# Kernel tuning notes

Hardware: AMD Instinct MI355X
Metric: run time of the kernel (lower is better)

## Reference

```python
import jax, jax.numpy as jnp
import numpy as np

D_IN = 1024
D_OUT = 1024
NUM_HEADS = 16
HEAD_DIM = D_OUT // NUM_HEADS


def setup_inputs() -> dict:
    key = jax.random.key(0)
    ks = jax.random.split(key, 6)
    s = 0.02
    return {
        "x": jax.random.normal(ks[0], (4, 2048, D_IN), dtype=jnp.float32),
        "Wq": jax.random.normal(ks[1], (D_IN, D_OUT), dtype=jnp.float32) * s,
        "Wk": jax.random.normal(ks[2], (D_IN, D_OUT), dtype=jnp.float32) * s,
        "Wv": jax.random.normal(ks[3], (D_IN, D_OUT), dtype=jnp.float32) * s,
        "Wo": jax.random.normal(ks[4], (D_OUT, D_OUT), dtype=jnp.float32) * s,
        "bo": jax.random.normal(ks[5], (D_OUT,), dtype=jnp.float32) * s,
    }


def reference(x, Wq, Wk, Wv, Wo, bo):
    b, n, _ = x.shape
    h, hd = NUM_HEADS, HEAD_DIM
    # project and split heads: (b, h, n, hd)
    q = (x @ Wq).reshape(b, n, h, hd).transpose(0, 2, 1, 3)
    k = (x @ Wk).reshape(b, n, h, hd).transpose(0, 2, 1, 3)
    v = (x @ Wv).reshape(b, n, h, hd).transpose(0, 2, 1, 3)
    scores = jnp.einsum("bhqd,bhkd->bhqk", q, k)
    causal = jnp.triu(jnp.ones((n, n), dtype=bool), k=1)  # True above diagonal
    scores = jnp.where(causal, -jnp.inf, scores)
    attn = jax.nn.softmax(scores / jnp.sqrt(jnp.float32(hd)), axis=-1)
    ctx = jnp.einsum("bhqk,bhkd->bhqd", attn, v)
    ctx = ctx.transpose(0, 2, 1, 3).reshape(b, n, h * hd)
    return ctx @ Wo + bo
```

## Files before the change

### kernel.cpp

```cpp
#include <hip/hip_runtime.h>

#define DEV __device__ __forceinline__

typedef unsigned short u16;
typedef unsigned int u32;
typedef __attribute__((ext_vector_type(8))) short short8;
typedef __attribute__((ext_vector_type(4))) float floatx4;

DEV u16 f2bf(float f) {
  union { float f; unsigned u; } v; v.f = f;
  return (u16)((v.u + 0x7FFFu + ((v.u >> 16) & 1u)) >> 16);
}
DEV u32 fbits(float f) { union { float f; u32 u; } v; v.f = f; return v.u; }

DEV void gl2lds16(const void* g, void* l) {
  __builtin_amdgcn_global_load_lds((const __attribute__((address_space(1))) void*)g,
                                   (__attribute__((address_space(3))) void*)l, 16, 0, 0);
}

__global__ void cvt_f32_bf16_x4(const float* __restrict__ in, u16* __restrict__ out, int n4) {
  int i = blockIdx.x * blockDim.x + threadIdx.x;
  if (i >= n4) return;
  float4 f = ((const float4*)in)[i];
  ushort4 o;
  o.x = f2bf(f.x); o.y = f2bf(f.y); o.z = f2bf(f.z); o.w = f2bf(f.w);
  ((ushort4*)out)[i] = o;
}

__global__ void transpose_f32_bf16(const float* __restrict__ W, u16* __restrict__ Wt) {
  __shared__ float t[32][33];
  int tx = threadIdx.x & 31, ty = threadIdx.x >> 5;
  int x0 = blockIdx.x * 32, y0 = blockIdx.y * 32;
#pragma unroll
  for (int i = 0; i < 32; i += 8)
    t[ty + i][tx] = W[(size_t)(y0 + ty + i) * 1024 + x0 + tx];
  __syncthreads();
#pragma unroll
  for (int i = 0; i < 32; i += 8)
    Wt[(size_t)(x0 + ty + i) * 1024 + y0 + tx] = f2bf(t[tx][ty + i]);
}

__global__ __launch_bounds__(256, 4)
void gemm_qkv(const u16* __restrict__ A, const u16* __restrict__ Bt,
              u16* __restrict__ Qo, u16* __restrict__ Ko, u16* __restrict__ Vto,
              float alpha) {
  __shared__ u16 smem[16384];
  u16* As = smem;
  u16* Bs = smem + 8192;
  const int tid = threadIdx.x;
  const int wave = tid >> 6, lane = tid & 63;
  const int quad = lane >> 4, l16 = lane & 15, l7 = l16 & 7;
  const int n0 = blockIdx.x * 128, m0 = blockIdx.y * 128;
  const int wm = (wave >> 1) * 64, wn = (wave & 1) * 64;

  floatx4 acc[4][4] = {};
  const int sl = lane >> 3;
  const int sp = lane & 7;
  for (int kt = 0; kt < 1024; kt += 64) {
    __syncthreads();
#pragma unroll
    for (int it = 0; it < 4; ++it) {
      int g = it * 4 + wave;
      int row = g * 8 + sl;
      int lc = (sp ^ (row & 7)) * 8;
      gl2lds16(&A[(size_t)(m0 + row) * 1024 + kt + lc], &As[g * 512]);
      gl2lds16(&Bt[(size_t)(n0 + row) * 1024 + kt + lc], &Bs[g * 512]);
    }
    __syncthreads();
#pragma unroll
    for (int ks = 0; ks < 2; ++ks) {
      const int rc = ((ks * 4 + quad) ^ l7) * 8;
      short8 ar[4], br[4];
#pragma unroll
      for (int i = 0; i < 4; ++i)
        ar[i] = *(const short8*)&As[(wm + i * 16 + l16) * 64 + rc];
#pragma unroll
      for (int j = 0; j < 4; ++j)
        br[j] = *(const short8*)&Bs[(wn + j * 16 + l16) * 64 + rc];
#pragma unroll
      for (int i = 0; i < 4; ++i)
#pragma unroll
        for (int j = 0; j < 4; ++j)
          acc[i][j] = __builtin_amdgcn_mfma_f32_16x16x32_bf16(ar[i], br[j], acc[i][j], 0, 0, 0);
    }
  }

  if (n0 < 1024) {
#pragma unroll
    for (int i = 0; i < 4; ++i) {
      int row = m0 + wm + i * 16 + quad * 4;
#pragma unroll
      for (int j = 0; j < 4; ++j) {
        int col = n0 + wn + j * 16 + l16;
#pragma unroll
        for (int r = 0; r < 4; ++r)
          Qo[(size_t)(row + r) * 1024 + col] = f2bf(acc[i][j][r] * alpha);
      }
    }
  } else if (n0 < 2048) {
#pragma unroll
    for (int i = 0; i < 4; ++i) {
      int row = m0 + wm + i * 16 + quad * 4;
#pragma unroll
      for (int j = 0; j < 4; ++j) {
        int col = n0 - 1024 + wn + j * 16 + l16;
#pragma unroll
        for (int r = 0; r < 4; ++r)
          Ko[(size_t)(row + r) * 1024 + col] = f2bf(acc[i][j][r]);
      }
    }
  } else {
    __syncthreads();
#pragma unroll
    for (int i = 0; i < 4; ++i) {
      int rowrel0 = wm + i * 16 + quad * 4;
#pragma unroll
      for (int j = 0; j < 4; ++j) {
        int colrel = wn + j * 16 + l16;
        ushort4 pk;
        pk.x = f2bf(acc[i][j][0]); pk.y = f2bf(acc[i][j][1]);
        pk.z = f2bf(acc[i][j][2]); pk.w = f2bf(acc[i][j][3]);
        *(ushort4*)&smem[colrel * 128 + (rowrel0 ^ ((colrel & 15) * 8))] = pk;
      }
    }
    __syncthreads();
    const int bb = m0 >> 11, q0r = m0 & 2047;
    const int fl = tid >> 4, qp = (tid & 15) * 8;
#pragma unroll
    for (int p = 0; p < 8; ++p) {
      int f = p * 16 + fl;
      int col = n0 - 2048 + f;
      int h = col >> 6, d = col & 63;
      int sw = (f & 15) * 8;
      uint2 lo = *(const uint2*)&smem[f * 128 + (qp ^ sw)];
      uint2 hi = *(const uint2*)&smem[f * 128 + ((qp + 4) ^ sw)];
      uint4 val = make_uint4(lo.x, lo.y, hi.x, hi.y);
      *(uint4*)&Vto[(size_t)(((bb * 16 + h) * 64 + d)) * 2048 + q0r + qp] = val;
    }
  }
}

__global__ __launch_bounds__(256, 4)
void gemm_out(const u16* __restrict__ A, const u16* __restrict__ Bt,
              float* __restrict__ C, const float* __restrict__ bias) {
  __shared__ u16 smem[16384];
  u16* As = smem;
  u16* Bs = smem + 8192;
  const int tid = threadIdx.x;
  const int wave = tid >> 6, lane = tid & 63;
  const int quad = lane >> 4, l16 = lane & 15, l7 = l16 & 7;
  const int n0 = blockIdx.x * 128, m0 = blockIdx.y * 128;
  const int wm = (wave >> 1) * 64, wn = (wave & 1) * 64;

  floatx4 acc[4][4] = {};
  const int sl = lane >> 3;
  const int sp = lane & 7;

  for (int kt = 0; kt < 1024; kt += 64) {
    __syncthreads();
#pragma unroll
    for (int it = 0; it < 4; ++it) {
      int g = it * 4 + wave;
      int row = g * 8 + sl;
      int lc = (sp ^ (row & 7)) * 8;
      gl2lds16(&A[(size_t)(m0 + row) * 1024 + kt + lc], &As[g * 512]);
      gl2lds16(&Bt[(size_t)(n0 + row) * 1024 + kt + lc], &Bs[g * 512]);
    }
    __syncthreads();
#pragma unroll
    for (int ks = 0; ks < 2; ++ks) {
      const int rc = ((ks * 4 + quad) ^ l7) * 8;
      short8 ar[4], br[4];
#pragma unroll
      for (int i = 0; i < 4; ++i)
        ar[i] = *(const short8*)&As[(wm + i * 16 + l16) * 64 + rc];
#pragma unroll
      for (int j = 0; j < 4; ++j)
        br[j] = *(const short8*)&Bs[(wn + j * 16 + l16) * 64 + rc];
#pragma unroll
      for (int i = 0; i < 4; ++i)
#pragma unroll
        for (int j = 0; j < 4; ++j)
          acc[i][j] = __builtin_amdgcn_mfma_f32_16x16x32_bf16(ar[i], br[j], acc[i][j], 0, 0, 0);
    }
  }
#pragma unroll
  for (int j = 0; j < 4; ++j) {
    int col = n0 + wn + j * 16 + l16;
    float bj = bias[col];
#pragma unroll
    for (int i = 0; i < 4; ++i) {
      int row = m0 + wm + i * 16 + quad * 4;
#pragma unroll
      for (int r = 0; r < 4; ++r)
        C[(size_t)(row + r) * 1024 + col] = acc[i][j][r] + bj;
    }
  }
}

__global__ __launch_bounds__(256)
void flash_attn(const u16* __restrict__ Qg, const u16* __restrict__ Kg,
                const u16* __restrict__ Vtg, u16* __restrict__ ctx) {
  __shared__ u16 Qs[128 * 64];
  __shared__ u16 Ks[64 * 64];
  __shared__ u16 Vs[64 * 64];
  __shared__ u16 Ps[4][32 * 64];
  const int tid = threadIdx.x;
  const int wave = tid >> 6, lane = tid & 63;
  const int quad = lane >> 4, l16 = lane & 15, l7 = l16 & 7;
  const int bh = blockIdx.y, b = bh >> 4, h = bh & 15;
  const size_t qkbase = (size_t)b * 2048 * 1024 + (size_t)h * 64;
  const size_t vbase = (size_t)bh * 64 * 2048;
  const int sl = lane >> 3, sp = lane & 7;
  u16* Pw = &Ps[wave][0];

  for (int phase = 0; phase < 2; ++phase) {
    const int qt = phase == 0 ? (15 - (int)blockIdx.x) : (int)blockIdx.x;
    const int q0 = qt * 128;
    __syncthreads();
    {
#pragma unroll
      for (int it = 0; it < 4; ++it) {
        int g = it * 4 + wave;
        int r = g * 8 + sl;
        int lc = (sp ^ (r & 7)) * 8;
        gl2lds16(&Qg[qkbase + (size_t)(q0 + r) * 1024 + lc], &Qs[g * 512]);
      }
    }
    float lsum[2] = {0.f, 0.f};
    floatx4 o[4][2] = {};

    const int qbase = q0 + wave * 32;
    const int nt = 2 * qt + 2;

    for (int t = 0; t < nt; ++t) {
      const int kv0 = t * 64;
      __syncthreads();
      {
#pragma unroll
        for (int it = 0; it < 2; ++it) {
          int g = it * 4 + wave;
          int r = g * 8 + sl;
          int lc = (sp ^ (r & 7)) * 8;
          gl2lds16(&Kg[qkbase + (size_t)(kv0 + r) * 1024 + lc], &Ks[g * 512]);
          gl2lds16(&Vtg[vbase + (size_t)r * 2048 + kv0 + lc], &Vs[g * 512]);
        }
      }
      __syncthreads();

      if (kv0 > qbase + 31) continue;

      floatx4 st[4][2] = {};
#pragma unroll
      for (int ks = 0; ks < 2; ++ks) {
        const int rc = ((ks * 4 + quad) ^ l7) * 8;
        short8 ak[4], bq[2];
#pragma unroll
        for (int mj = 0; mj < 4; ++mj)
          ak[mj] = *(const short8*)&Ks[(mj * 16 + l16) * 64 + rc];
#pragma unroll
        for (int qi = 0; qi < 2; ++qi)
          bq[qi] = *(const short8*)&Qs[(wave * 32 + qi * 16 + l16) * 64 + rc];
#pragma unroll
        for (int mj = 0; mj < 4; ++mj)
#pragma unroll
          for (int qi = 0; qi < 2; ++qi)
            st[mj][qi] = __builtin_amdgcn_mfma_f32_16x16x32_bf16(ak[mj], bq[qi], st[mj][qi], 0, 0, 0);
      }
#pragma unroll
      for (int mj = 0; mj < 4; ++mj)
#pragma unroll
        for (int qi = 0; qi < 2; ++qi)
#pragma unroll
          for (int r = 0; r < 4; ++r)
            st[mj][qi][r] = __builtin_amdgcn_exp2f(st[mj][qi][r]);
      if (kv0 + 63 > qbase) {
#pragma unroll
        for (int mj = 0; mj < 4; ++mj)
#pragma unroll
          for (int r = 0; r < 4; ++r) {
            int gk = kv0 + mj * 16 + quad * 4 + r;
#pragma unroll
            for (int qi = 0; qi < 2; ++qi) {
              int gq = qbase + qi * 16 + l16;
              if (gk > gq) st[mj][qi][r] = 0.f;
            }
          }
      }
#pragma unroll
      for (int mj = 0; mj < 4; ++mj)
#pragma unroll
        for (int qi = 0; qi < 2; ++qi)
          lsum[qi] += (st[mj][qi][0] + st[mj][qi][1]) + (st[mj][qi][2] + st[mj][qi][3]);
#pragma unroll
      for (int qi = 0; qi < 2; ++qi) {
        int rowoff = (qi * 16 + l16) * 64;
#pragma unroll
        for (int mj = 0; mj < 4; ++mj) {
          u32 lo = __builtin_amdgcn_perm(fbits(st[mj][qi][1]), fbits(st[mj][qi][0]), 0x07060302u);
          u32 hi = __builtin_amdgcn_perm(fbits(st[mj][qi][3]), fbits(st[mj][qi][2]), 0x07060302u);
          int off = rowoff + (((mj * 2 + (quad >> 1)) ^ l7) << 3) + (quad & 1) * 4;
          *(uint2*)&Pw[off] = make_uint2(lo, hi);
        }
      }
#pragma unroll
      for (int ks = 0; ks < 2; ++ks) {
        const int rc = ((ks * 4 + quad) ^ l7) * 8;
        short8 av[4], bp[2];
#pragma unroll
        for (int dj = 0; dj < 4; ++dj)
          av[dj] = *(const short8*)&Vs[(dj * 16 + l16) * 64 + rc];
#pragma unroll
        for (int qi = 0; qi < 2; ++qi)
          bp[qi] = *(const short8*)&Pw[(qi * 16 + l16) * 64 + rc];
#pragma unroll
        for (int dj = 0; dj < 4; ++dj)
#pragma unroll
          for (int qi = 0; qi < 2; ++qi)
            o[dj][qi] = __builtin_amdgcn_mfma_f32_16x16x32_bf16(av[dj], bp[qi], o[dj][qi], 0, 0, 0);
      }
    }
#pragma unroll
    for (int qi = 0; qi < 2; ++qi) {
      float tsum = lsum[qi];
      tsum += __shfl_xor(tsum, 16);
      tsum += __shfl_xor(tsum, 32);
      float inv = 1.f / tsum;
      int gq = qbase + qi * 16 + l16;
      size_t rowoff = ((size_t)b * 2048 + gq) * 1024 + (size_t)h * 64 + quad * 4;
#pragma unroll
      for (int dj = 0; dj < 4; ++dj) {
        ushort4 pk;
        pk.x = f2bf(o[dj][qi][0] * inv); pk.y = f2bf(o[dj][qi][1] * inv);
        pk.z = f2bf(o[dj][qi][2] * inv); pk.w = f2bf(o[dj][qi][3] * inv);
        *(ushort4*)&ctx[rowoff + dj * 16] = pk;
      }
    }
  }
}

extern "C" void kernel_launch(void* const* d_in, const int* in_sizes, int n_in,
                              void* d_out, int out_size, void* d_ws, size_t ws_size,
                              hipStream_t stream) {
  const float* x  = (const float*)d_in[0];
  const float* Wq = (const float*)d_in[1];
  const float* Wk = (const float*)d_in[2];
  const float* Wv = (const float*)d_in[3];
  const float* Wo = (const float*)d_in[4];
  const float* bo = (const float*)d_in[5];
  float* out = (float*)d_out;

  char* ws = (char*)d_ws;
  const size_t MB = (size_t)1 << 20;
  u16* x16    = (u16*)(ws + 0 * MB);
  u16* q16    = (u16*)(ws + 16 * MB);
  u16* k16    = (u16*)(ws + 32 * MB);
  u16* vt16   = (u16*)(ws + 48 * MB);
  u16* c16    = (u16*)(ws + 64 * MB);
  u16* wqkvt  = (u16*)(ws + 80 * MB);
  u16* wot    = (u16*)(ws + 86 * MB);

  const float sc2 = 0.125f * 1.44269504089f;

  cvt_f32_bf16_x4<<<8192, 256, 0, stream>>>(x, x16, 8192 * 1024 / 4);
  dim3 tg(32, 32);
  transpose_f32_bf16<<<tg, 256, 0, stream>>>(Wq, wqkvt);
  transpose_f32_bf16<<<tg, 256, 0, stream>>>(Wk, wqkvt + (size_t)1024 * 1024);
  transpose_f32_bf16<<<tg, 256, 0, stream>>>(Wv, wqkvt + (size_t)2048 * 1024);
  transpose_f32_bf16<<<tg, 256, 0, stream>>>(Wo, wot);

  dim3 g3(3072 / 128, 8192 / 128);
  gemm_qkv<<<g3, 256, 0, stream>>>(x16, wqkvt, q16, k16, vt16, sc2);

  dim3 ag(8, 64);
  flash_attn<<<ag, 256, 0, stream>>>(q16, k16, vt16, c16);

  dim3 gO(1024 / 128, 8192 / 128);
  gemm_out<<<gO, 256, 0, stream>>>(c16, wot, out, bo);
}
```

Baseline: 259.3 us.

## Use 128-wide KV tiles in flash attention and remap block indices for locality

Doubles the K/V tile from 64 to 128 keys per iteration, halving the number of load/sync rounds per query tile and computing 8 score subtiles per step. The V tile gets a wider 16-way XOR swizzle, and P is written and consumed in two 64-key halves through the existing per-wave LDS buffer. The 1D grid is remapped so neighbouring blocks share batch-heads, launch bounds request 2 blocks per CU, and the per-wave skip of fully masked tiles is dropped. In exchange, each wave now does some fully masked work on the diagonal tile, and LDS and register use rise.

```diff
diff --git a/kernel.cpp b/kernel.cpp
--- a/kernel.cpp
+++ b/kernel.cpp
@@ -198,24 +198,28 @@
   }
 }
 
-__global__ __launch_bounds__(256)
+__global__ __launch_bounds__(256, 2)
 void flash_attn(const u16* __restrict__ Qg, const u16* __restrict__ Kg,
                 const u16* __restrict__ Vtg, u16* __restrict__ ctx) {
   __shared__ u16 Qs[128 * 64];
-  __shared__ u16 Ks[64 * 64];
-  __shared__ u16 Vs[64 * 64];
+  __shared__ u16 Ks[128 * 64];
+  __shared__ u16 Vs[64 * 128];
   __shared__ u16 Ps[4][32 * 64];
   const int tid = threadIdx.x;
   const int wave = tid >> 6, lane = tid & 63;
   const int quad = lane >> 4, l16 = lane & 15, l7 = l16 & 7;
-  const int bh = blockIdx.y, b = bh >> 4, h = bh & 15;
+  const int bx = blockIdx.x;
+  const int p = (bx >> 3) & 7;
+  const int bh = (bx >> 6) * 8 + (bx & 7);
+  const int b = bh >> 4, h = bh & 15;
   const size_t qkbase = (size_t)b * 2048 * 1024 + (size_t)h * 64;
   const size_t vbase = (size_t)bh * 64 * 2048;
   const int sl = lane >> 3, sp = lane & 7;
+  const int sv = lane >> 4, sq = lane & 15;
   u16* Pw = &Ps[wave][0];
 
   for (int phase = 0; phase < 2; ++phase) {
-    const int qt = phase == 0 ? (15 - (int)blockIdx.x) : (int)blockIdx.x;
+    const int qt = phase == 0 ? (15 - p) : p;
     const int q0 = qt * 128;
     __syncthreads();
     {
@@ -231,52 +235,49 @@
     floatx4 o[4][2] = {};
 
     const int qbase = q0 + wave * 32;
-    const int nt = 2 * qt + 2;
+    const int nt = qt + 1;
 
     for (int t = 0; t < nt; ++t) {
-      const int kv0 = t * 64;
+      const int kv0 = t * 128;
       __syncthreads();
       {
 #pragma unroll
-        for (int it = 0; it < 2; ++it) {
+        for (int it = 0; it < 4; ++it) {
           int g = it * 4 + wave;
-          int r = g * 8 + sl;
-          int lc = (sp ^ (r & 7)) * 8;
-          gl2lds16(&Kg[qkbase + (size_t)(kv0 + r) * 1024 + lc], &Ks[g * 512]);
-          gl2lds16(&Vtg[vbase + (size_t)r * 2048 + kv0 + lc], &Vs[g * 512]);
+          int rk = g * 8 + sl;
+          int lck = (sp ^ (rk & 7)) * 8;
+          gl2lds16(&Kg[qkbase + (size_t)(kv0 + rk) * 1024 + lck], &Ks[g * 512]);
+          int rv = g * 4 + sv;
+          int lcv = (sq ^ (rv & 15)) * 8;
+          gl2lds16(&Vtg[vbase + (size_t)rv * 2048 + kv0 + lcv], &Vs[g * 512]);
         }
       }
       __syncthreads();
 
-      if (kv0 > qbase + 31) continue;
-
-      floatx4 st[4][2] = {};
+      floatx4 st[8][2] = {};
 #pragma unroll
       for (int ks = 0; ks < 2; ++ks) {
         const int rc = ((ks * 4 + quad) ^ l7) * 8;
-        short8 ak[4], bq[2];
-#pragma unroll
-        for (int mj = 0; mj < 4; ++mj)
-          ak[mj] = *(const short8*)&Ks[(mj * 16 + l16) * 64 + rc];
-#pragma unroll
-        for (int qi = 0; qi < 2; ++qi)
-          bq[qi] = *(const short8*)&Qs[(wave * 32 + qi * 16 + l16) * 64 + rc];
-#pragma unroll
-        for (int mj = 0; mj < 4; ++mj)
-#pragma unroll
-          for (int qi = 0; qi < 2; ++qi)
-            st[mj][qi] = __builtin_amdgcn_mfma_f32_16x16x32_bf16(ak[mj], bq[qi], st[mj][qi], 0, 0, 0);
-      }
-#pragma unroll
-      for (int mj = 0; mj < 4; ++mj)
+        short8 bq[2];
+        bq[0] = *(const short8*)&Qs[(wave * 32 + l16) * 64 + rc];
+        bq[1] = *(const short8*)&Qs[(wave * 32 + 16 + l16) * 64 + rc];
+#pragma unroll
+        for (int mj = 0; mj < 8; ++mj) {
+          short8 ak = *(const short8*)&Ks[(mj * 16 + l16) * 64 + rc];
+          st[mj][0] = __builtin_amdgcn_mfma_f32_16x16x32_bf16(ak, bq[0], st[mj][0], 0, 0, 0);
+          st[mj][1] = __builtin_amdgcn_mfma_f32_16x16x32_bf16(ak, bq[1], st[mj][1], 0, 0, 0);
+        }
+      }
+#pragma unroll
+      for (int mj = 0; mj < 8; ++mj)
 #pragma unroll
         for (int qi = 0; qi < 2; ++qi)
 #pragma unroll
           for (int r = 0; r < 4; ++r)
             st[mj][qi][r] = __builtin_amdgcn_exp2f(st[mj][qi][r]);
-      if (kv0 + 63 > qbase) {
-#pragma unroll
-        for (int mj = 0; mj < 4; ++mj)
+      if (t == nt - 1) {
+#pragma unroll
+        for (int mj = 0; mj < 8; ++mj)
 #pragma unroll
           for (int r = 0; r < 4; ++r) {
             int gk = kv0 + mj * 16 + quad * 4 + r;
@@ -288,36 +289,42 @@
           }
       }
 #pragma unroll
-      for (int mj = 0; mj < 4; ++mj)
+      for (int mj = 0; mj < 8; ++mj)
 #pragma unroll
         for (int qi = 0; qi < 2; ++qi)
           lsum[qi] += (st[mj][qi][0] + st[mj][qi][1]) + (st[mj][qi][2] + st[mj][qi][3]);
 #pragma unroll
-      for (int qi = 0; qi < 2; ++qi) {
-        int rowoff = (qi * 16 + l16) * 64;
-#pragma unroll
-        for (int mj = 0; mj < 4; ++mj) {
-          u32 lo = __builtin_amdgcn_perm(fbits(st[mj][qi][1]), fbits(st[mj][qi][0]), 0x07060302u);
-          u32 hi = __builtin_amdgcn_perm(fbits(st[mj][qi][3]), fbits(st[mj][qi][2]), 0x07060302u);
-          int off = rowoff + (((mj * 2 + (quad >> 1)) ^ l7) << 3) + (quad & 1) * 4;
-          *(uint2*)&Pw[off] = make_uint2(lo, hi);
+      for (int half = 0; half < 2; ++half) {
+#pragma unroll
+        for (int qi = 0; qi < 2; ++qi) {
+          int rowoff = (qi * 16 + l16) * 64;
+#pragma unroll
+          for (int mj2 = 0; mj2 < 4; ++mj2) {
+            int mj = half * 4 + mj2;
+            u32 lo = __builtin_amdgcn_perm(fbits(st[mj][qi][1]), fbits(st[mj][qi][0]), 0x07060302u);
+            u32 hi = __builtin_amdgcn_perm(fbits(st[mj][qi][3]), fbits(st[mj][qi][2]), 0x07060302u);
+            int off = rowoff + (((mj2 * 2 + (quad >> 1)) ^ l7) << 3) + (quad & 1) * 4;
+            *(uint2*)&Pw[off] = make_uint2(lo, hi);
+          }
         }
-      }
-#pragma unroll
-      for (int ks = 0; ks < 2; ++ks) {
-        const int rc = ((ks * 4 + quad) ^ l7) * 8;
-        short8 av[4], bp[2];
-#pragma unroll
-        for (int dj = 0; dj < 4; ++dj)
-          av[dj] = *(const short8*)&Vs[(dj * 16 + l16) * 64 + rc];
-#pragma unroll
-        for (int qi = 0; qi < 2; ++qi)
-          bp[qi] = *(const short8*)&Pw[(qi * 16 + l16) * 64 + rc];
-#pragma unroll
-        for (int dj = 0; dj < 4; ++dj)
+#pragma unroll
+        for (int ks2 = 0; ks2 < 2; ++ks2) {
+          const int ks = half * 2 + ks2;
+          const int rcv = ((ks * 4 + quad) ^ l16) * 8;
+          const int rcp = ((ks2 * 4 + quad) ^ l7) * 8;
+          short8 av[4], bp[2];
+#pragma unroll
+          for (int dj = 0; dj < 4; ++dj)
+            av[dj] = *(const short8*)&Vs[(dj * 16 + l16) * 128 + rcv];
 #pragma unroll
           for (int qi = 0; qi < 2; ++qi)
-            o[dj][qi] = __builtin_amdgcn_mfma_f32_16x16x32_bf16(av[dj], bp[qi], o[dj][qi], 0, 0, 0);
+            bp[qi] = *(const short8*)&Pw[(qi * 16 + l16) * 64 + rcp];
+#pragma unroll
+          for (int dj = 0; dj < 4; ++dj)
+#pragma unroll
+            for (int qi = 0; qi < 2; ++qi)
+              o[dj][qi] = __builtin_amdgcn_mfma_f32_16x16x32_bf16(av[dj], bp[qi], o[dj][qi], 0, 0, 0);
+        }
       }
     }
 #pragma unroll
@@ -372,8 +379,7 @@
   dim3 g3(3072 / 128, 8192 / 128);
   gemm_qkv<<<g3, 256, 0, stream>>>(x16, wqkvt, q16, k16, vt16, sc2);
 
-  dim3 ag(8, 64);
-  flash_attn<<<ag, 256, 0, stream>>>(q16, k16, vt16, c16);
+  flash_attn<<<512, 256, 0, stream>>>(q16, k16, vt16, c16);
 
   dim3 gO(1024 / 128, 8192 / 128);
   gemm_out<<<gO, 256, 0, stream>>>(c16, wot, out, bo);
```

Result: faster. 231.2 us (-10.8%).

## Double-buffer K/V tiles in flash attention and keep Q fragments in registers

Applied to the files above, without the earlier changes.

Each K/V tile is now prefetched into a second LDS buffer while the current tile is processed. This removes one barrier per iteration and hides global-load latency behind the MFMA work. Q is staged once through the P scratch area and held in registers for the whole phase, so total LDS stays the same and Q is no longer re-read from LDS. The grid becomes 1D with a remapped block index so neighbouring blocks share heads, and launch bounds request three blocks per CU. That cap can force register spills given the extra live Q fragments and accumulators.

```diff
diff --git a/kernel.cpp b/kernel.cpp
--- a/kernel.cpp
+++ b/kernel.cpp
@@ -198,25 +198,31 @@
   }
 }
 
-__global__ __launch_bounds__(256)
+__global__ __launch_bounds__(256, 3)
 void flash_attn(const u16* __restrict__ Qg, const u16* __restrict__ Kg,
                 const u16* __restrict__ Vtg, u16* __restrict__ ctx) {
-  __shared__ u16 Qs[128 * 64];
-  __shared__ u16 Ks[64 * 64];
-  __shared__ u16 Vs[64 * 64];
+  __shared__ u16 Ks[2][64 * 64];
+  __shared__ u16 Vs[2][64 * 64];
   __shared__ u16 Ps[4][32 * 64];
   const int tid = threadIdx.x;
   const int wave = tid >> 6, lane = tid & 63;
   const int quad = lane >> 4, l16 = lane & 15, l7 = l16 & 7;
-  const int bh = blockIdx.y, b = bh >> 4, h = bh & 15;
+  const int bx = blockIdx.x;
+  const int p = (bx >> 3) & 7;
+  const int bh = (bx >> 6) * 8 + (bx & 7);
+  const int b = bh >> 4, h = bh & 15;
   const size_t qkbase = (size_t)b * 2048 * 1024 + (size_t)h * 64;
   const size_t vbase = (size_t)bh * 64 * 2048;
   const int sl = lane >> 3, sp = lane & 7;
   u16* Pw = &Ps[wave][0];
+  u16* Qsc = &Ps[0][0];
 
   for (int phase = 0; phase < 2; ++phase) {
-    const int qt = phase == 0 ? (15 - (int)blockIdx.x) : (int)blockIdx.x;
+    const int qt = phase == 0 ? (15 - p) : p;
     const int q0 = qt * 128;
+    const int qbase = q0 + wave * 32;
+    const int nt = 2 * qt + 2;
+
     __syncthreads();
     {
 #pragma unroll
@@ -224,48 +230,59 @@
         int g = it * 4 + wave;
         int r = g * 8 + sl;
         int lc = (sp ^ (r & 7)) * 8;
-        gl2lds16(&Qg[qkbase + (size_t)(q0 + r) * 1024 + lc], &Qs[g * 512]);
-      }
-    }
+        gl2lds16(&Qg[qkbase + (size_t)(q0 + r) * 1024 + lc], &Qsc[g * 512]);
+      }
+#pragma unroll
+      for (int it = 0; it < 2; ++it) {
+        int g = it * 4 + wave;
+        int r = g * 8 + sl;
+        int lc = (sp ^ (r & 7)) * 8;
+        gl2lds16(&Kg[qkbase + (size_t)r * 1024 + lc], &Ks[0][g * 512]);
+        gl2lds16(&Vtg[vbase + (size_t)r * 2048 + lc], &Vs[0][g * 512]);
+      }
+    }
+    __syncthreads();
+
+    short8 bq[2][2];
+#pragma unroll
+    for (int ks = 0; ks < 2; ++ks) {
+      const int rc = ((ks * 4 + quad) ^ l7) * 8;
+      bq[ks][0] = *(const short8*)&Qsc[(wave * 32 + l16) * 64 + rc];
+      bq[ks][1] = *(const short8*)&Qsc[(wave * 32 + 16 + l16) * 64 + rc];
+    }
+
     float lsum[2] = {0.f, 0.f};
     floatx4 o[4][2] = {};
 
-    const int qbase = q0 + wave * 32;
-    const int nt = 2 * qt + 2;
-
     for (int t = 0; t < nt; ++t) {
       const int kv0 = t * 64;
-      __syncthreads();
-      {
+      if (t > 0) __syncthreads();
+      if (t + 1 < nt) {
+        const int kvn = kv0 + 64;
+        const int bn = (t + 1) & 1;
 #pragma unroll
         for (int it = 0; it < 2; ++it) {
           int g = it * 4 + wave;
           int r = g * 8 + sl;
           int lc = (sp ^ (r & 7)) * 8;
-          gl2lds16(&Kg[qkbase + (size_t)(kv0 + r) * 1024 + lc], &Ks[g * 512]);
-          gl2lds16(&Vtg[vbase + (size_t)r * 2048 + kv0 + lc], &Vs[g * 512]);
+          gl2lds16(&Kg[qkbase + (size_t)(kvn + r) * 1024 + lc], &Ks[bn][g * 512]);
+          gl2lds16(&Vtg[vbase + (size_t)r * 2048 + kvn + lc], &Vs[bn][g * 512]);
         }
       }
-      __syncthreads();
-
       if (kv0 > qbase + 31) continue;
 
+      const u16* Kb = &Ks[t & 1][0];
+      const u16* Vb = &Vs[t & 1][0];
       floatx4 st[4][2] = {};
 #pragma unroll
       for (int ks = 0; ks < 2; ++ks) {
         const int rc = ((ks * 4 + quad) ^ l7) * 8;
-        short8 ak[4], bq[2];
-#pragma unroll
-        for (int mj = 0; mj < 4; ++mj)
-          ak[mj] = *(const short8*)&Ks[(mj * 16 + l16) * 64 + rc];
-#pragma unroll
-        for (int qi = 0; qi < 2; ++qi)
-          bq[qi] = *(const short8*)&Qs[(wave * 32 + qi * 16 + l16) * 64 + rc];
-#pragma unroll
-        for (int mj = 0; mj < 4; ++mj)
-#pragma unroll
-          for (int qi = 0; qi < 2; ++qi)
-            st[mj][qi] = __builtin_amdgcn_mfma_f32_16x16x32_bf16(ak[mj], bq[qi], st[mj][qi], 0, 0, 0);
+#pragma unroll
+        for (int mj = 0; mj < 4; ++mj) {
+          short8 ak = *(const short8*)&Kb[(mj * 16 + l16) * 64 + rc];
+          st[mj][0] = __builtin_amdgcn_mfma_f32_16x16x32_bf16(ak, bq[ks][0], st[mj][0], 0, 0, 0);
+          st[mj][1] = __builtin_amdgcn_mfma_f32_16x16x32_bf16(ak, bq[ks][1], st[mj][1], 0, 0, 0);
+        }
       }
 #pragma unroll
       for (int mj = 0; mj < 4; ++mj)
@@ -309,7 +326,7 @@
         short8 av[4], bp[2];
 #pragma unroll
         for (int dj = 0; dj < 4; ++dj)
-          av[dj] = *(const short8*)&Vs[(dj * 16 + l16) * 64 + rc];
+          av[dj] = *(const short8*)&Vb[(dj * 16 + l16) * 64 + rc];
 #pragma unroll
         for (int qi = 0; qi < 2; ++qi)
           bp[qi] = *(const short8*)&Pw[(qi * 16 + l16) * 64 + rc];
@@ -372,8 +389,7 @@
   dim3 g3(3072 / 128, 8192 / 128);
   gemm_qkv<<<g3, 256, 0, stream>>>(x16, wqkvt, q16, k16, vt16, sc2);
 
-  dim3 ag(8, 64);
-  flash_attn<<<ag, 256, 0, stream>>>(q16, k16, vt16, c16);
+  flash_attn<<<512, 256, 0, stream>>>(q16, k16, vt16, c16);
 
   dim3 gO(1024 / 128, 8192 / 128);
   gemm_out<<<gO, 256, 0, stream>>>(c16, wot, out, bo);
```

New measurement: 243.6 us. -6.0%, faster.
